# Kernel optimization log

Measured on AMD Instinct MI355X. Metric: run time of the kernel, lower is better.

The kernel has to match this reference:

```python
import jax, jax.numpy as jnp
import numpy as np

B, F, M, D, VE, H, V = 16, 4096, 512, 256, 64, 512, 50
OUT = 8  # 4 * 2


def setup_inputs() -> dict:
    key = jax.random.key(0)
    ks = jax.random.split(key, 10)
    features = jax.random.normal(ks[0], (B, F, D), dtype=jnp.float32)
    vowels = jax.random.randint(ks[1], (B, M), 0, V)
    # frames of a mora are contiguous -> sorted indices per utterance
    mora_index = jnp.sort(jax.random.randint(ks[2], (B, F), 0, M), axis=-1)
    emb_table = jax.random.normal(ks[3], (V, VE), dtype=jnp.float32) * 0.02
    W_mora = jax.random.normal(ks[4], (D + VE, H), dtype=jnp.float32) / np.sqrt(D + VE)
    b_mora = jnp.zeros((H,), jnp.float32)
    W_frame = jax.random.normal(ks[5], (D, H), dtype=jnp.float32) / np.sqrt(D)
    b_frame = jnp.zeros((H,), jnp.float32)
    W_post = jax.random.normal(ks[6], (H, OUT), dtype=jnp.float32) / np.sqrt(H)
    b_post = jnp.zeros((OUT,), jnp.float32)
    return {
        "vowels": vowels, "features": features, "mora_index": mora_index,
        "emb_table": emb_table, "W_mora": W_mora, "b_mora": b_mora,
        "W_frame": W_frame, "b_frame": b_frame, "W_post": W_post, "b_post": b_post,
    }


def _segment_mean(features, mora_index):
    # features: [B, F, D]; mora_index: [B, F] in [0, M)
    b, f, d = features.shape
    flat_idx = (mora_index + jnp.arange(b)[:, None] * M).reshape(-1)  # [B*F]
    flat = features.reshape(b * f, d)
    sums = jax.ops.segment_sum(flat, flat_idx, num_segments=b * M)  # [B*M, D]
    cnt = jax.ops.segment_sum(jnp.ones((b * f,), features.dtype), flat_idx,
                              num_segments=b * M)[:, None]
    # scatter_reduce(mean, include_self=False): empty segments stay 0
    mean = jnp.where(cnt > 0, sums / jnp.maximum(cnt, 1.0), 0.0)
    return mean.reshape(b, M, d)


def reference(vowels, features, mora_index, emb_table, W_mora, b_mora,
              W_frame, b_frame, W_post, b_post):
    mora_feat = _segment_mean(features, mora_index)          # [B, M, D]
    mv = emb_table[vowels]                                   # [B, M, VE]
    mh = jnp.concatenate([mv, mora_feat], axis=-1) @ W_mora + b_mora  # [B, M, H]
    fh = features @ W_frame + b_frame                        # [B, F, H] (frame branch; encoder = identity on mora stream)
    del fh
    out = mh @ W_post + b_post                               # [B, M, 8]
    return out.reshape(out.shape[0], out.shape[1], 2, 4)
```

## Files before the change

### kernel.cpp

```cpp
#include <hip/hip_runtime.h>

#define B_DIM  16
#define F_DIM  4096
#define M_DIM  512
#define D_DIM  256
#define VE_DIM 64
#define H_DIM  512
#define K_DIM  320
#define OUT_DIM 8

__global__ __launch_bounds__(256) void prep_kernel(
    const float* __restrict__ W_mora,
    const float* __restrict__ b_mora,
    const float* __restrict__ W_post,
    const float* __restrict__ b_post,
    const int* __restrict__ mora_index,
    float* __restrict__ WcT,
    float* __restrict__ bc,
    int* __restrict__ seg)
{
    const int blk = blockIdx.x;
    const int tid = threadIdx.x;
    if (blk < 642) {
        const int w    = blk * 4 + (tid >> 6);
        const int lane = tid & 63;
        float sum = 0.f;
        if (w < 2560) {
            const int k = w >> 3, o = w & 7;
            const float* arow = W_mora + k * H_DIM;
            #pragma unroll
            for (int it = 0; it < H_DIM / 64; ++it) {
                const int j = lane + it * 64;
                sum += arow[j] * W_post[j * OUT_DIM + o];
            }
            #pragma unroll
            for (int off = 32; off >= 1; off >>= 1) sum += __shfl_down(sum, off, 64);
            if (lane == 0) WcT[o * K_DIM + k] = sum;
        } else {
            const int o = w - 2560;
            #pragma unroll
            for (int it = 0; it < H_DIM / 64; ++it) {
                const int j = lane + it * 64;
                sum += b_mora[j] * W_post[j * OUT_DIM + o];
            }
            #pragma unroll
            for (int off = 32; off >= 1; off >>= 1) sum += __shfl_down(sum, off, 64);
            if (lane == 0) bc[o] = sum + b_post[o];
        }
    } else {
        const int t = (blk - 642) * 256 + tid;
        const int b = t >> 12;
        const int f = t & (F_DIM - 1);
        const int* mi = mora_index + b * F_DIM;
        const int cur = mi[f];
        int* sg = seg + b * (M_DIM + 1);
        if (f == 0) {
            for (int m = 0; m <= cur; ++m) sg[m] = 0;
        } else {
            const int prev = mi[f - 1];
            for (int m = prev + 1; m <= cur; ++m) sg[m] = f;
        }
        if (f == F_DIM - 1) {
            for (int m = cur + 1; m <= M_DIM; ++m) sg[m] = F_DIM;
        }
    }
}

__global__ __launch_bounds__(256) void main_kernel(
    const int* __restrict__ vowels,
    const float* __restrict__ features,
    const float* __restrict__ emb,
    const float* __restrict__ WcT,
    const float* __restrict__ bc,
    const int* __restrict__ seg,
    float* __restrict__ out)
{
    __shared__ float sWcT[OUT_DIM * K_DIM];
    __shared__ float sbc[OUT_DIM];
    __shared__ float sx[K_DIM];
    __shared__ __align__(16) float sred[4 * 256];
    __shared__ float spart[4 * OUT_DIM];
    __shared__ int   sbounds[9];

    const int b   = blockIdx.x >> 6;
    const int m0  = (blockIdx.x & 63) * 8;
    const int tid = threadIdx.x;
    const int lane = tid & 63;
    const int wv   = tid >> 6;

    for (int i = tid; i < OUT_DIM * K_DIM; i += 256) sWcT[i] = WcT[i];
    if (tid < OUT_DIM) sbc[tid] = bc[tid];
    if (tid < 9) sbounds[tid] = seg[b * (M_DIM + 1) + m0 + tid];
    __syncthreads();

    const float4* feat4 = (const float4*)features + (size_t)b * F_DIM * (D_DIM / 4);
    const int q = lane;
    const int g = wv;

    for (int mm = 0; mm < 8; ++mm) {
        const int fs = sbounds[mm], fe = sbounds[mm + 1];
        const int cnt = fe - fs;

        float a0 = 0.f, a1 = 0.f, a2 = 0.f, a3 = 0.f;
        for (int f = fs + g; f < fe; f += 4) {
            const float4 v = feat4[f * 64 + q];
            a0 += v.x; a1 += v.y; a2 += v.z; a3 += v.w;
        }
        *(float4*)&sred[g * 256 + q * 4] = make_float4(a0, a1, a2, a3);
        __syncthreads();

        const float inv = (cnt > 0) ? 1.0f / (float)cnt : 0.0f;
        const float s = sred[tid] + sred[256 + tid] + sred[512 + tid] + sred[768 + tid];
        sx[VE_DIM + tid] = s * inv;
        if (tid < VE_DIM) {
            const int vw = vowels[b * M_DIM + m0 + mm];
            sx[tid] = emb[vw * VE_DIM + tid];
        }
        __syncthreads();

        float p[OUT_DIM];
        {
            const float xk = sx[tid];
            #pragma unroll
            for (int o = 0; o < OUT_DIM; ++o) p[o] = xk * sWcT[o * K_DIM + tid];
            if (tid < 64) {
                const float xk2 = sx[256 + tid];
                #pragma unroll
                for (int o = 0; o < OUT_DIM; ++o) p[o] += xk2 * sWcT[o * K_DIM + 256 + tid];
            }
        }
        #pragma unroll
        for (int off = 32; off >= 1; off >>= 1) {
            #pragma unroll
            for (int o = 0; o < OUT_DIM; ++o) p[o] += __shfl_down(p[o], off, 64);
        }
        if (lane == 0) {
            #pragma unroll
            for (int o = 0; o < OUT_DIM; ++o) spart[wv * OUT_DIM + o] = p[o];
        }
        __syncthreads();
        if (tid < OUT_DIM) {
            const float r = spart[tid] + spart[8 + tid] + spart[16 + tid] + spart[24 + tid]
                          + sbc[tid];
            out[(size_t)(b * M_DIM + m0 + mm) * OUT_DIM + tid] = r;
        }
        __syncthreads();
    }
}

extern "C" void kernel_launch(void* const* d_in, const int* in_sizes, int n_in,
                              void* d_out, int out_size, void* d_ws, size_t ws_size,
                              hipStream_t stream) {
    const int*   vowels     = (const int*)d_in[0];
    const float* features   = (const float*)d_in[1];
    const int*   mora_index = (const int*)d_in[2];
    const float* emb        = (const float*)d_in[3];
    const float* W_mora     = (const float*)d_in[4];
    const float* b_mora     = (const float*)d_in[5];
    const float* W_post     = (const float*)d_in[8];
    const float* b_post     = (const float*)d_in[9];
    float*       out        = (float*)d_out;

    float* WcT = (float*)d_ws;
    float* bc  = WcT + OUT_DIM * K_DIM;
    int*   seg = (int*)(bc + OUT_DIM);

    prep_kernel<<<642 + (B_DIM * F_DIM) / 256, 256, 0, stream>>>(
        W_mora, b_mora, W_post, b_post, mora_index, WcT, bc, seg);
    main_kernel<<<(B_DIM * M_DIM) / 8, 256, 0, stream>>>(
        vowels, features, emb, WcT, bc, seg, out);
}
```

Baseline: 135.4 us.

## Split frame range evenly across waves with LDS atomics, fewer morae per block

The main kernel now gives each block 4 morae instead of 8. Each wave takes a contiguous, equal share of the block's frame range and accumulates per-mora partial sums, flushing them to shared memory with atomicAdd at segment boundaries. Loads are unrolled by 8 to keep more memory requests in flight. The per-mora projection is done by one wave each, which removes most of the block-wide barriers. The cost is LDS atomic traffic, extra branching at boundaries, and twice as many blocks, each reloading the combined weight matrix.

New measurement: 133.5 us. Within noise of the previous version (-1.4%).

```diff
diff --git a/kernel.cpp b/kernel.cpp
--- a/kernel.cpp
+++ b/kernel.cpp
@@ -8,6 +8,8 @@
 #define H_DIM  512
 #define K_DIM  320
 #define OUT_DIM 8
+#define MPB    4
+#define UNROLL 8
 
 __global__ __launch_bounds__(256) void prep_kernel(
     const float* __restrict__ W_mora,
@@ -36,7 +38,7 @@
             #pragma unroll
             for (int off = 32; off >= 1; off >>= 1) sum += __shfl_down(sum, off, 64);
             if (lane == 0) WcT[o * K_DIM + k] = sum;
-        } else {
+        } else if (w < 2568) {
             const int o = w - 2560;
             #pragma unroll
             for (int it = 0; it < H_DIM / 64; ++it) {
@@ -76,58 +78,87 @@
     float* __restrict__ out)
 {
     __shared__ float sWcT[OUT_DIM * K_DIM];
+    __shared__ float sums[MPB][D_DIM];
     __shared__ float sbc[OUT_DIM];
-    __shared__ float sx[K_DIM];
-    __shared__ __align__(16) float sred[4 * 256];
-    __shared__ float spart[4 * OUT_DIM];
-    __shared__ int   sbounds[9];
+    __shared__ int   sbounds[MPB + 1];
 
-    const int b   = blockIdx.x >> 6;
-    const int m0  = (blockIdx.x & 63) * 8;
-    const int tid = threadIdx.x;
+    const int b    = blockIdx.x >> 7;
+    const int m0   = (blockIdx.x & 127) * MPB;
+    const int tid  = threadIdx.x;
     const int lane = tid & 63;
     const int wv   = tid >> 6;
 
-    for (int i = tid; i < OUT_DIM * K_DIM; i += 256) sWcT[i] = WcT[i];
+    for (int i = tid; i < OUT_DIM * K_DIM / 4; i += 256)
+        ((float4*)sWcT)[i] = ((const float4*)WcT)[i];
     if (tid < OUT_DIM) sbc[tid] = bc[tid];
-    if (tid < 9) sbounds[tid] = seg[b * (M_DIM + 1) + m0 + tid];
+    if (tid <= MPB) sbounds[tid] = seg[b * (M_DIM + 1) + m0 + tid];
+    for (int i = tid; i < MPB * D_DIM; i += 256) ((float*)sums)[i] = 0.f;
     __syncthreads();
 
     const float4* feat4 = (const float4*)features + (size_t)b * F_DIM * (D_DIM / 4);
-    const int q = lane;
-    const int g = wv;
+    const int fs0 = sbounds[0], fe = sbounds[MPB];
+    const int len = fe - fs0;
+    const int s_g = fs0 + ((len * wv) >> 2);
+    const int e_g = fs0 + ((len * (wv + 1)) >> 2);
 
-    for (int mm = 0; mm < 8; ++mm) {
-        const int fs = sbounds[mm], fe = sbounds[mm + 1];
-        const int cnt = fe - fs;
-
+    if (s_g < e_g) {
+        int mm = 0;
+        while (sbounds[mm + 1] <= s_g) ++mm;
         float a0 = 0.f, a1 = 0.f, a2 = 0.f, a3 = 0.f;
-        for (int f = fs + g; f < fe; f += 4) {
-            const float4 v = feat4[f * 64 + q];
+        int f = s_g;
+        for (; f + UNROLL <= e_g; f += UNROLL) {
+            float4 v[UNROLL];
+            #pragma unroll
+            for (int i = 0; i < UNROLL; ++i)
+                v[i] = feat4[(size_t)(f + i) * 64 + lane];
+            #pragma unroll
+            for (int i = 0; i < UNROLL; ++i) {
+                const int ff = f + i;
+                if (ff >= sbounds[mm + 1]) {
+                    atomicAdd(&sums[mm][lane * 4 + 0], a0);
+                    atomicAdd(&sums[mm][lane * 4 + 1], a1);
+                    atomicAdd(&sums[mm][lane * 4 + 2], a2);
+                    atomicAdd(&sums[mm][lane * 4 + 3], a3);
+                    a0 = a1 = a2 = a3 = 0.f;
+                    do { ++mm; } while (sbounds[mm + 1] <= ff);
+                }
+                a0 += v[i].x; a1 += v[i].y; a2 += v[i].z; a3 += v[i].w;
+            }
+        }
+        for (; f < e_g; ++f) {
+            const float4 v = feat4[(size_t)f * 64 + lane];
+            if (f >= sbounds[mm + 1]) {
+                atomicAdd(&sums[mm][lane * 4 + 0], a0);
+                atomicAdd(&sums[mm][lane * 4 + 1], a1);
+                atomicAdd(&sums[mm][lane * 4 + 2], a2);
+                atomicAdd(&sums[mm][lane * 4 + 3], a3);
+                a0 = a1 = a2 = a3 = 0.f;
+                do { ++mm; } while (sbounds[mm + 1] <= f);
+            }
             a0 += v.x; a1 += v.y; a2 += v.z; a3 += v.w;
         }
-        *(float4*)&sred[g * 256 + q * 4] = make_float4(a0, a1, a2, a3);
-        __syncthreads();
+        atomicAdd(&sums[mm][lane * 4 + 0], a0);
+        atomicAdd(&sums[mm][lane * 4 + 1], a1);
+        atomicAdd(&sums[mm][lane * 4 + 2], a2);
+        atomicAdd(&sums[mm][lane * 4 + 3], a3);
+    }
+    __syncthreads();
 
+    {
+        const int m   = m0 + wv;
+        const int cnt = sbounds[wv + 1] - sbounds[wv];
         const float inv = (cnt > 0) ? 1.0f / (float)cnt : 0.0f;
-        const float s = sred[tid] + sred[256 + tid] + sred[512 + tid] + sred[768 + tid];
-        sx[VE_DIM + tid] = s * inv;
-        if (tid < VE_DIM) {
-            const int vw = vowels[b * M_DIM + m0 + mm];
-            sx[tid] = emb[vw * VE_DIM + tid];
-        }
-        __syncthreads();
-
+        const int vw  = vowels[b * M_DIM + m];
         float p[OUT_DIM];
-        {
-            const float xk = sx[tid];
+        const float x0 = emb[vw * VE_DIM + lane];
+        #pragma unroll
+        for (int o = 0; o < OUT_DIM; ++o) p[o] = x0 * sWcT[o * K_DIM + lane];
+        #pragma unroll
+        for (int j = 1; j < 5; ++j) {
+            const int k = lane + 64 * j;
+            const float x = sums[wv][k - VE_DIM] * inv;
             #pragma unroll
-            for (int o = 0; o < OUT_DIM; ++o) p[o] = xk * sWcT[o * K_DIM + tid];
-            if (tid < 64) {
-                const float xk2 = sx[256 + tid];
-                #pragma unroll
-                for (int o = 0; o < OUT_DIM; ++o) p[o] += xk2 * sWcT[o * K_DIM + 256 + tid];
-            }
+            for (int o = 0; o < OUT_DIM; ++o) p[o] += x * sWcT[o * K_DIM + k];
         }
         #pragma unroll
         for (int off = 32; off >= 1; off >>= 1) {
@@ -136,15 +167,9 @@
         }
         if (lane == 0) {
             #pragma unroll
-            for (int o = 0; o < OUT_DIM; ++o) spart[wv * OUT_DIM + o] = p[o];
+            for (int o = 0; o < OUT_DIM; ++o)
+                out[(size_t)(b * M_DIM + m) * OUT_DIM + o] = p[o] + sbc[o];
         }
-        __syncthreads();
-        if (tid < OUT_DIM) {
-            const float r = spart[tid] + spart[8 + tid] + spart[16 + tid] + spart[24 + tid]
-                          + sbc[tid];
-            out[(size_t)(b * M_DIM + m0 + mm) * OUT_DIM + tid] = r;
-        }
-        __syncthreads();
     }
 }
 
@@ -167,6 +192,6 @@
 
     prep_kernel<<<642 + (B_DIM * F_DIM) / 256, 256, 0, stream>>>(
         W_mora, b_mora, W_post, b_post, mora_index, WcT, bc, seg);
-    main_kernel<<<(B_DIM * M_DIM) / 8, 256, 0, stream>>>(
+    main_kernel<<<(B_DIM * M_DIM) / MPB, 256, 0, stream>>>(
         vowels, features, emb, WcT, bc, seg, out);
 }
```

## Replace per-mora gather with frame-parallel atomic segment sums and separate finish kernel

Applied to the files above, without the earlier changes.

Instead of each block walking the frames of 8 morae using precomputed segment bounds, a new kernel assigns each wavefront 16 contiguous frames, accumulates runs of equal mora index in registers, and flushes partial sums and counts to a zeroed workspace with float atomics. A separate finish kernel computes the mean and applies the folded 320x8 projection using register-resident weights and xor shuffles, with no shared memory or barriers. This spreads the 64 MB feature read evenly across the GPU regardless of segment length, at the cost of an extra launch, zeroing 8 MB of workspace, a global round trip for the sums, and atomic traffic where runs cross chunk boundaries.

Result: slower. 157.6 us (+16.4%).

```diff
diff --git a/kernel.cpp b/kernel.cpp
--- a/kernel.cpp
+++ b/kernel.cpp
@@ -9,19 +9,23 @@
 #define K_DIM  320
 #define OUT_DIM 8
 
+#define NMORA        (B_DIM * M_DIM)
+#define SUMS_FLOATS  (NMORA * D_DIM)
+#define FOLD_BLOCKS  642
+#define ZBLOCKS      514
+
 __global__ __launch_bounds__(256) void prep_kernel(
     const float* __restrict__ W_mora,
     const float* __restrict__ b_mora,
     const float* __restrict__ W_post,
     const float* __restrict__ b_post,
-    const int* __restrict__ mora_index,
     float* __restrict__ WcT,
     float* __restrict__ bc,
-    int* __restrict__ seg)
+    float* __restrict__ zero_base)
 {
     const int blk = blockIdx.x;
     const int tid = threadIdx.x;
-    if (blk < 642) {
+    if (blk < FOLD_BLOCKS) {
         const int w    = blk * 4 + (tid >> 6);
         const int lane = tid & 63;
         float sum = 0.f;
@@ -36,7 +40,7 @@
             #pragma unroll
             for (int off = 32; off >= 1; off >>= 1) sum += __shfl_down(sum, off, 64);
             if (lane == 0) WcT[o * K_DIM + k] = sum;
-        } else {
+        } else if (w < 2568) {
             const int o = w - 2560;
             #pragma unroll
             for (int it = 0; it < H_DIM / 64; ++it) {
@@ -48,103 +52,122 @@
             if (lane == 0) bc[o] = sum + b_post[o];
         }
     } else {
-        const int t = (blk - 642) * 256 + tid;
-        const int b = t >> 12;
-        const int f = t & (F_DIM - 1);
-        const int* mi = mora_index + b * F_DIM;
-        const int cur = mi[f];
-        int* sg = seg + b * (M_DIM + 1);
-        if (f == 0) {
-            for (int m = 0; m <= cur; ++m) sg[m] = 0;
-        } else {
-            const int prev = mi[f - 1];
-            for (int m = prev + 1; m <= cur; ++m) sg[m] = f;
-        }
-        if (f == F_DIM - 1) {
-            for (int m = cur + 1; m <= M_DIM; ++m) sg[m] = F_DIM;
-        }
+        const int zb = blk - FOLD_BLOCKS;
+        float4* z = (float4*)zero_base;
+        #pragma unroll
+        for (int j = 0; j < 4; ++j)
+            z[zb * 1024 + j * 256 + tid] = make_float4(0.f, 0.f, 0.f, 0.f);
     }
 }
 
-__global__ __launch_bounds__(256) void main_kernel(
+__device__ __forceinline__ void flush_run(float* __restrict__ sums,
+                                          float* __restrict__ cnt,
+                                          int gm, const float4& a, int n, int lane)
+{
+    float* base = sums + (size_t)gm * D_DIM + lane * 4;
+    atomicAdd(base + 0, a.x);
+    atomicAdd(base + 1, a.y);
+    atomicAdd(base + 2, a.z);
+    atomicAdd(base + 3, a.w);
+    if (lane == 0) atomicAdd(cnt + gm, (float)n);
+}
+
+__global__ __launch_bounds__(256) void seg_sum_kernel(
+    const float* __restrict__ features,
+    const int* __restrict__ mora_index,
+    float* __restrict__ sums,
+    float* __restrict__ cnt)
+{
+    const int gw   = blockIdx.x * 4 + (threadIdx.x >> 6);
+    const int lane = threadIdx.x & 63;
+    const int b    = gw >> 8;
+    const int f0   = (gw & 255) * 16;
+
+    const int* mi = mora_index + b * F_DIM + f0;
+    int idx[16];
+    #pragma unroll
+    for (int i = 0; i < 16; ++i) idx[i] = mi[i];
+
+    const float4* src = (const float4*)features + ((size_t)b * F_DIM + f0) * 64 + lane;
+
+    float4 a = make_float4(0.f, 0.f, 0.f, 0.f);
+    int cur = idx[0];
+    int n = 0;
+    #pragma unroll
+    for (int h = 0; h < 2; ++h) {
+        float4 v[8];
+        #pragma unroll
+        for (int i = 0; i < 8; ++i) v[i] = src[(h * 8 + i) * 64];
+        #pragma unroll
+        for (int i = 0; i < 8; ++i) {
+            const int id = idx[h * 8 + i];
+            if (id != cur) {
+                flush_run(sums, cnt, b * M_DIM + cur, a, n, lane);
+                a = make_float4(0.f, 0.f, 0.f, 0.f);
+                n = 0;
+                cur = id;
+            }
+            a.x += v[i].x; a.y += v[i].y; a.z += v[i].z; a.w += v[i].w;
+            ++n;
+        }
+    }
+    flush_run(sums, cnt, b * M_DIM + cur, a, n, lane);
+}
+
+__global__ __launch_bounds__(256) void finish_kernel(
     const int* __restrict__ vowels,
-    const float* __restrict__ features,
     const float* __restrict__ emb,
     const float* __restrict__ WcT,
     const float* __restrict__ bc,
-    const int* __restrict__ seg,
+    const float* __restrict__ sums,
+    const float* __restrict__ cnt,
     float* __restrict__ out)
 {
-    __shared__ float sWcT[OUT_DIM * K_DIM];
-    __shared__ float sbc[OUT_DIM];
-    __shared__ float sx[K_DIM];
-    __shared__ __align__(16) float sred[4 * 256];
-    __shared__ float spart[4 * OUT_DIM];
-    __shared__ int   sbounds[9];
+    const int lane   = threadIdx.x & 63;
+    const int wv     = threadIdx.x >> 6;
+    const int m_base = blockIdx.x * 32 + wv * 8;
 
-    const int b   = blockIdx.x >> 6;
-    const int m0  = (blockIdx.x & 63) * 8;
-    const int tid = threadIdx.x;
-    const int lane = tid & 63;
-    const int wv   = tid >> 6;
-
-    for (int i = tid; i < OUT_DIM * K_DIM; i += 256) sWcT[i] = WcT[i];
-    if (tid < OUT_DIM) sbc[tid] = bc[tid];
-    if (tid < 9) sbounds[tid] = seg[b * (M_DIM + 1) + m0 + tid];
-    __syncthreads();
-
-    const float4* feat4 = (const float4*)features + (size_t)b * F_DIM * (D_DIM / 4);
-    const int q = lane;
-    const int g = wv;
+    float Wm[OUT_DIM][4], We[OUT_DIM][4];
+    #pragma unroll
+    for (int o = 0; o < OUT_DIM; ++o) {
+        const float4 t = *(const float4*)&WcT[o * K_DIM + VE_DIM + lane * 4];
+        Wm[o][0] = t.x; Wm[o][1] = t.y; Wm[o][2] = t.z; Wm[o][3] = t.w;
+        const float4 u = *(const float4*)&WcT[o * K_DIM + (lane & 15) * 4];
+        We[o][0] = u.x; We[o][1] = u.y; We[o][2] = u.z; We[o][3] = u.w;
+    }
+    float bcr[OUT_DIM];
+    #pragma unroll
+    for (int o = 0; o < OUT_DIM; ++o) bcr[o] = bc[o];
 
     for (int mm = 0; mm < 8; ++mm) {
-        const int fs = sbounds[mm], fe = sbounds[mm + 1];
-        const int cnt = fe - fs;
-
-        float a0 = 0.f, a1 = 0.f, a2 = 0.f, a3 = 0.f;
-        for (int f = fs + g; f < fe; f += 4) {
-            const float4 v = feat4[f * 64 + q];
-            a0 += v.x; a1 += v.y; a2 += v.z; a3 += v.w;
-        }
-        *(float4*)&sred[g * 256 + q * 4] = make_float4(a0, a1, a2, a3);
-        __syncthreads();
-
-        const float inv = (cnt > 0) ? 1.0f / (float)cnt : 0.0f;
-        const float s = sred[tid] + sred[256 + tid] + sred[512 + tid] + sred[768 + tid];
-        sx[VE_DIM + tid] = s * inv;
-        if (tid < VE_DIM) {
-            const int vw = vowels[b * M_DIM + m0 + mm];
-            sx[tid] = emb[vw * VE_DIM + tid];
-        }
-        __syncthreads();
+        const int gm = m_base + mm;
+        const float4 s = *(const float4*)&sums[(size_t)gm * D_DIM + lane * 4];
+        const float c = cnt[gm];
+        const float inv = (c > 0.f) ? 1.0f / c : 0.0f;
+        const int vw = vowels[gm];
 
         float p[OUT_DIM];
-        {
-            const float xk = sx[tid];
+        #pragma unroll
+        for (int o = 0; o < OUT_DIM; ++o)
+            p[o] = (s.x * Wm[o][0] + s.y * Wm[o][1] + s.z * Wm[o][2] + s.w * Wm[o][3]) * inv;
+
+        if (lane < 16) {
+            const float4 e = *(const float4*)&emb[vw * VE_DIM + lane * 4];
             #pragma unroll
-            for (int o = 0; o < OUT_DIM; ++o) p[o] = xk * sWcT[o * K_DIM + tid];
-            if (tid < 64) {
-                const float xk2 = sx[256 + tid];
-                #pragma unroll
-                for (int o = 0; o < OUT_DIM; ++o) p[o] += xk2 * sWcT[o * K_DIM + 256 + tid];
-            }
+            for (int o = 0; o < OUT_DIM; ++o)
+                p[o] += e.x * We[o][0] + e.y * We[o][1] + e.z * We[o][2] + e.w * We[o][3];
         }
+
         #pragma unroll
         for (int off = 32; off >= 1; off >>= 1) {
             #pragma unroll
-            for (int o = 0; o < OUT_DIM; ++o) p[o] += __shfl_down(p[o], off, 64);
+            for (int o = 0; o < OUT_DIM; ++o) p[o] += __shfl_xor(p[o], off, 64);
         }
         if (lane == 0) {
-            #pragma unroll
-            for (int o = 0; o < OUT_DIM; ++o) spart[wv * OUT_DIM + o] = p[o];
+            float4* o4 = (float4*)(out + (size_t)gm * OUT_DIM);
+            o4[0] = make_float4(p[0] + bcr[0], p[1] + bcr[1], p[2] + bcr[2], p[3] + bcr[3]);
+            o4[1] = make_float4(p[4] + bcr[4], p[5] + bcr[5], p[6] + bcr[6], p[7] + bcr[7]);
         }
-        __syncthreads();
-        if (tid < OUT_DIM) {
-            const float r = spart[tid] + spart[8 + tid] + spart[16 + tid] + spart[24 + tid]
-                          + sbc[tid];
-            out[(size_t)(b * M_DIM + m0 + mm) * OUT_DIM + tid] = r;
-        }
-        __syncthreads();
     }
 }
 
@@ -161,12 +184,13 @@
     const float* b_post     = (const float*)d_in[9];
     float*       out        = (float*)d_out;
 
-    float* WcT = (float*)d_ws;
-    float* bc  = WcT + OUT_DIM * K_DIM;
-    int*   seg = (int*)(bc + OUT_DIM);
+    float* sums = (float*)d_ws;
+    float* cnt  = sums + SUMS_FLOATS;
+    float* WcT  = cnt + NMORA;
+    float* bc   = WcT + OUT_DIM * K_DIM;
 
-    prep_kernel<<<642 + (B_DIM * F_DIM) / 256, 256, 0, stream>>>(
-        W_mora, b_mora, W_post, b_post, mora_index, WcT, bc, seg);
-    main_kernel<<<(B_DIM * M_DIM) / 8, 256, 0, stream>>>(
-        vowels, features, emb, WcT, bc, seg, out);
+    prep_kernel<<<FOLD_BLOCKS + ZBLOCKS, 256, 0, stream>>>(
+        W_mora, b_mora, W_post, b_post, WcT, bc, sums );
+    seg_sum_kernel<<<1024, 256, 0, stream>>>(features, mora_index, sums, cnt);
+    finish_kernel<<<256, 256, 0, stream>>>(vowels, emb, WcT, bc, sums, cnt, out);
 }
```
